# Performance work log

Hardware: AMD Instinct MI355X
Metric: run time of the kernel (lower is better)

The kernel has to match this reference:

```python
import jax, jax.numpy as jnp
import numpy as np

B, N, IN_DIM, HID, OUT, HEADS = 2, 1024, 64, 64, 64, 4
PHD1, PHD2 = HID // HEADS, OUT // HEADS
SLOPE = 0.2  # PyG GATv2Conv default negative_slope
EPS = 1e-12  # F.normalize eps


def _gatv2_dense(x, Wl, Wr, att, bias, heads, phd, mask):
    """Dense GATv2 layer over a full adjacency mask.
    x: [B,N,Din]; Wl/Wr: [Din, heads*phd]; att: [heads,phd]; bias: [heads*phd];
    mask: [N,N] bool, mask[i,j]=True means edge j->i exists.
    """
    Bb, Nn, _ = x.shape
    xl = (x @ Wl).reshape(Bb, Nn, heads, phd)  # source features
    xr = (x @ Wr).reshape(Bb, Nn, heads, phd)  # target features
    # s[b,i,j,h,p] = leaky_relu(xr[b,i] + xl[b,j])  (GATv2)
    s = jax.nn.leaky_relu(xr[:, :, None] + xl[:, None, :], SLOPE)
    e = jnp.einsum('bijhp,hp->bijh', s, att)  # [B,Ni,Nj,H]
    e = jnp.where(mask[None, :, :, None], e, -jnp.inf)
    alpha = jax.nn.softmax(e, axis=2)  # softmax over source nodes j
    out = jnp.einsum('bijh,bjhp->bihp', alpha, xl).reshape(Bb, Nn, heads * phd)
    return out + bias


def setup_inputs() -> dict:
    key = jax.random.key(0)
    ks = jax.random.split(key, 10)
    sc = 0.1
    return {
        'x': jax.random.normal(ks[0], (B, N, IN_DIM), jnp.float32),
        'embedding': jax.random.normal(ks[1], (N, HID), jnp.float32),
        'Wl1': jax.random.normal(ks[2], (IN_DIM, HEADS * PHD1), jnp.float32) * sc,
        'Wr1': jax.random.normal(ks[3], (IN_DIM, HEADS * PHD1), jnp.float32) * sc,
        'att1': jax.random.normal(ks[4], (HEADS, PHD1), jnp.float32) * sc,
        'b1': jnp.zeros((HEADS * PHD1,), jnp.float32),
        'Wl2': jax.random.normal(ks[5], (HID, HEADS * PHD2), jnp.float32) * sc,
        'Wr2': jax.random.normal(ks[6], (HID, HEADS * PHD2), jnp.float32) * sc,
        'att2': jax.random.normal(ks[7], (HEADS, PHD2), jnp.float32) * sc,
        'b2': jnp.zeros((HEADS * PHD2,), jnp.float32),
    }


def reference(x, embedding, Wl1, Wr1, att1, b1, Wl2, Wr2, att2, b2):
    # AdaptiveAdjacency: cosine-similarity adjacency; only its nonzero pattern is used.
    norm = jnp.maximum(jnp.linalg.norm(embedding, axis=1, keepdims=True), EPS)
    ne = embedding / norm
    adj = ne @ ne.T  # [N,N]
    # edge set = adj.nonzero(); GATv2Conv(add_self_loops=True) guarantees diagonal
    mask = (adj != 0) | jnp.eye(N, dtype=bool)
    h = jax.nn.relu(_gatv2_dense(x, Wl1, Wr1, att1, b1, HEADS, PHD1, mask))
    # dropout(0.3) in eval mode -> identity
    return _gatv2_dense(h, Wl2, Wr2, att2, b2, HEADS, PHD2, mask)
```

## Files before the change

### kernel.cpp

```cpp
#include <hip/hip_runtime.h>
#include <math.h>

#define NN 1024
#define BB 2
#define D 64
#define NHEAD 4
#define LOG2E 1.4426950408889634f
#define MST 65

template <int CTRL>
__device__ __forceinline__ float dpp_mov(float x) {
    int xi = __builtin_bit_cast(int, x);
    int r = __builtin_amdgcn_update_dpp(0, xi, CTRL, 0xF, 0xF, true);
    return __builtin_bit_cast(float, r);
}

__device__ __forceinline__ float dpp_rowsum16(float t) {
    t += dpp_mov<0x111>(t);
    t += dpp_mov<0x112>(t);
    t += dpp_mov<0x114>(t);
    t += dpp_mov<0x118>(t);
    return t;
}

__global__ __launch_bounds__(256) void k_mask_gemm(
    const float* __restrict__ emb, unsigned char* __restrict__ mask,
    const float* __restrict__ A, const float* __restrict__ Wl,
    const float* __restrict__ Wr, const float* __restrict__ att,
    float* __restrict__ xl, float* __restrict__ xr, float* __restrict__ alE)
{
    __shared__ float SH[64 * MST * 2];
    int tid = threadIdx.x;
    if (blockIdx.x < 256) {
        float* As = SH;
        float* Bs = SH + 64 * MST;
        int ib = (blockIdx.x & 15) << 6;
        int jb = (blockIdx.x >> 4) << 6;

        #pragma unroll
        for (int r = 0; r < 4; ++r) {
            int q = tid + (r << 8);
            int row = q >> 4, c4 = (q & 15) << 2;
            float4 a = *(const float4*)&emb[(ib + row) * D + c4];
            float4 b = *(const float4*)&emb[(jb + row) * D + c4];
            As[row * MST + c4 + 0] = a.x; As[row * MST + c4 + 1] = a.y;
            As[row * MST + c4 + 2] = a.z; As[row * MST + c4 + 3] = a.w;
            Bs[row * MST + c4 + 0] = b.x; Bs[row * MST + c4 + 1] = b.y;
            Bs[row * MST + c4 + 2] = b.z; Bs[row * MST + c4 + 3] = b.w;
        }
        __syncthreads();

        int i0 = (tid >> 4) << 2;
        int j0 = (tid & 15) << 2;
        float acc[4][4] = {};
        #pragma unroll 8
        for (int k = 0; k < 64; ++k) {
            float a0 = As[(i0 + 0) * MST + k];
            float a1 = As[(i0 + 1) * MST + k];
            float a2 = As[(i0 + 2) * MST + k];
            float a3 = As[(i0 + 3) * MST + k];
            float b0 = Bs[(j0 + 0) * MST + k];
            float b1 = Bs[(j0 + 1) * MST + k];
            float b2 = Bs[(j0 + 2) * MST + k];
            float b3 = Bs[(j0 + 3) * MST + k];
            acc[0][0] = fmaf(a0, b0, acc[0][0]); acc[0][1] = fmaf(a0, b1, acc[0][1]);
            acc[0][2] = fmaf(a0, b2, acc[0][2]); acc[0][3] = fmaf(a0, b3, acc[0][3]);
            acc[1][0] = fmaf(a1, b0, acc[1][0]); acc[1][1] = fmaf(a1, b1, acc[1][1]);
            acc[1][2] = fmaf(a1, b2, acc[1][2]); acc[1][3] = fmaf(a1, b3, acc[1][3]);
            acc[2][0] = fmaf(a2, b0, acc[2][0]); acc[2][1] = fmaf(a2, b1, acc[2][1]);
            acc[2][2] = fmaf(a2, b2, acc[2][2]); acc[2][3] = fmaf(a2, b3, acc[2][3]);
            acc[3][0] = fmaf(a3, b0, acc[3][0]); acc[3][1] = fmaf(a3, b1, acc[3][1]);
            acc[3][2] = fmaf(a3, b2, acc[3][2]); acc[3][3] = fmaf(a3, b3, acc[3][3]);
        }
        #pragma unroll
        for (int r = 0; r < 4; ++r) {
            int gi = ib + i0 + r;
            uchar4 m;
            m.x = (acc[r][0] != 0.f || gi == jb + j0 + 0) ? 1 : 0;
            m.y = (acc[r][1] != 0.f || gi == jb + j0 + 1) ? 1 : 0;
            m.z = (acc[r][2] != 0.f || gi == jb + j0 + 2) ? 1 : 0;
            m.w = (acc[r][3] != 0.f || gi == jb + j0 + 3) ? 1 : 0;
            *(uchar4*)&mask[gi * NN + jb + j0] = m;
        }
    } else {
        float* wl = SH;
        float* wr = SH + 4096;
        for (int t = tid; t < 4096; t += 256) { wl[t] = Wl[t]; wr[t] = Wr[t]; }
        __syncthreads();
        int r = (blockIdx.x - 256) * 4 + (tid >> 6);
        int c = tid & 63;
        float av = att[c];
        const float* arow = A + r * 64;
        float accl = 0.f, accr = 0.f;
        #pragma unroll
        for (int p = 0; p < 64; ++p) {
            float a = arow[p];
            accl = fmaf(a, wl[p * 64 + c], accl);
            accr = fmaf(a, wr[p * 64 + c], accr);
        }
        int cp = (((c >> 2) & 3) << 4) | ((c >> 4) << 2) | (c & 3);
        xl[r * 64 + cp] = accl;
        xr[r * 64 + c] = accr;
        float t = dpp_rowsum16(accl * av);
        if ((c & 15) == 15) alE[(r << 2) | (c >> 4)] = 0.6f * LOG2E * t;
    }
}

__global__ __launch_bounds__(256) void k_gemm2(const float* __restrict__ A,
                                               const float* __restrict__ Wl,
                                               const float* __restrict__ Wr,
                                               const float* __restrict__ att,
                                               float* __restrict__ xl,
                                               float* __restrict__ xr,
                                               float* __restrict__ alE) {
    __shared__ float wl[64 * 64];
    __shared__ float wr[64 * 64];
    int tid = threadIdx.x;
    for (int t = tid; t < 4096; t += 256) { wl[t] = Wl[t]; wr[t] = Wr[t]; }
    __syncthreads();
    int r = blockIdx.x * 4 + (tid >> 6);
    int c = tid & 63;
    float av = att[c];
    const float* arow = A + r * 64;
    float accl = 0.f, accr = 0.f;
    #pragma unroll
    for (int p = 0; p < 64; ++p) {
        float a = arow[p];
        accl = fmaf(a, wl[p * 64 + c], accl);
        accr = fmaf(a, wr[p * 64 + c], accr);
    }
    int cp = (((c >> 2) & 3) << 4) | ((c >> 4) << 2) | (c & 3);
    xl[r * 64 + cp] = accl;
    xr[r * 64 + c] = accr;
    float t = dpp_rowsum16(accl * av);
    if ((c & 15) == 15) alE[(r << 2) | (c >> 4)] = 0.6f * LOG2E * t;
}

template <bool RELU>
__global__ __launch_bounds__(256, 2) void k_attn(
    const float* __restrict__ xlp, const float* __restrict__ xr,
    const float* __restrict__ att, const float* __restrict__ alE,
    const float* __restrict__ bias, const unsigned char* __restrict__ mask,
    float* __restrict__ out)
{
    __shared__ float Opart[4][4][4][64];
    __shared__ float Lpart[4][4][4][NHEAD];

    int tid = threadIdx.x;
    int wave = tid >> 6, lane = tid & 63;
    int h = lane & 3, jl = lane >> 2;
    int b = blockIdx.x >> 8;
    int i0 = (blockIdx.x & 255) << 2;
    int j0 = (wave << 8) + (jl << 4);

    const float* xlb = xlp + (b << 16);

    float at[16], xr0f[16], xr1f[16], xr2f[16], xr3f[16];
    {
        const float* ap = att + (h << 4);
        const float* r0 = xr + (((b << 10) + i0) << 6) + (h << 4);
        const float* r1 = r0 + 64;
        const float* r2 = r0 + 128;
        const float* r3 = r0 + 192;
        #pragma unroll
        for (int c = 0; c < 4; ++c) {
            *(float4*)&at[c << 2]   = *(const float4*)(ap + (c << 2));
            *(float4*)&xr0f[c << 2] = *(const float4*)(r0 + (c << 2));
            *(float4*)&xr1f[c << 2] = *(const float4*)(r1 + (c << 2));
            *(float4*)&xr2f[c << 2] = *(const float4*)(r2 + (c << 2));
            *(float4*)&xr3f[c << 2] = *(const float4*)(r3 + (c << 2));
        }
        #pragma unroll
        for (int p = 0; p < 16; ++p) at[p] *= 0.4f * LOG2E;
    }
    float ar0, ar1, ar2, ar3;
    {
        float s0[4], s1[4], s2[4], s3[4];
        #pragma unroll
        for (int c = 0; c < 4; ++c) {
            float t0 = 0.f, t1 = 0.f, t2 = 0.f, t3 = 0.f;
            #pragma unroll
            for (int r = 0; r < 4; ++r) {
                int p = (c << 2) + r;
                float a = at[p];
                t0 = fmaf(a, xr0f[p], t0);
                t1 = fmaf(a, xr1f[p], t1);
                t2 = fmaf(a, xr2f[p], t2);
                t3 = fmaf(a, xr3f[p], t3);
            }
            s0[c] = t0; s1[c] = t1; s2[c] = t2; s3[c] = t3;
        }
        ar0 = 1.5f * ((s0[0] + s0[1]) + (s0[2] + s0[3]));
        ar1 = 1.5f * ((s1[0] + s1[1]) + (s1[2] + s1[3]));
        ar2 = 1.5f * ((s2[0] + s2[1]) + (s2[2] + s2[3]));
        ar3 = 1.5f * ((s3[0] + s3[1]) + (s3[2] + s3[3]));
    }

    unsigned mb0 = 0, mb1 = 0, mb2 = 0, mb3 = 0;
    {
        const unsigned* m0p = (const unsigned*)(mask + (i0 + 0) * NN + j0);
        const unsigned* m1p = (const unsigned*)(mask + (i0 + 1) * NN + j0);
        const unsigned* m2p = (const unsigned*)(mask + (i0 + 2) * NN + j0);
        const unsigned* m3p = (const unsigned*)(mask + (i0 + 3) * NN + j0);
        #pragma unroll
        for (int q = 0; q < 4; ++q) {
            unsigned w0 = m0p[q], w1 = m1p[q], w2 = m2p[q], w3 = m3p[q];
            mb0 |= ((((w0 >> 0) & 1) | ((w0 >> 7) & 2) | ((w0 >> 14) & 4) | ((w0 >> 21) & 8)) << (q << 2));
            mb1 |= ((((w1 >> 0) & 1) | ((w1 >> 7) & 2) | ((w1 >> 14) & 4) | ((w1 >> 21) & 8)) << (q << 2));
            mb2 |= ((((w2 >> 0) & 1) | ((w2 >> 7) & 2) | ((w2 >> 14) & 4) | ((w2 >> 21) & 8)) << (q << 2));
            mb3 |= ((((w3 >> 0) & 1) | ((w3 >> 7) & 2) | ((w3 >> 14) & 4) | ((w3 >> 21) & 8)) << (q << 2));
        }
    }

    float O0[16], O1[16], O2[16], O3[16];
    float lq0 = 0.f, lq1 = 0.f, lq2 = 0.f, lq3 = 0.f;
    #pragma unroll
    for (int p = 0; p < 16; ++p) { O0[p] = 0.f; O1[p] = 0.f; O2[p] = 0.f; O3[p] = 0.f; }

    const float* xrow = xlb + (j0 << 6) + (h << 2);
    const float* alp  = alE + (b << 12) + (j0 << 2) + h;

    #pragma unroll 2
    for (int s = 0; s < 16; ++s) {
        const float* rp = xrow + (s << 6);
        float xv[16];
        *(float4*)&xv[0]  = *(const float4*)(rp);
        *(float4*)&xv[4]  = *(const float4*)(rp + 16);
        *(float4*)&xv[8]  = *(const float4*)(rp + 32);
        *(float4*)&xv[12] = *(const float4*)(rp + 48);
        float alr = alp[s << 2];
        bool m0 = (mb0 >> s) & 1, m1 = (mb1 >> s) & 1;
        bool m2 = (mb2 >> s) & 1, m3 = (mb3 >> s) & 1;

        float s0[4], s1[4], s2[4], s3[4];
        #pragma unroll
        for (int c = 0; c < 4; ++c) {
            float t0 = 0.f, t1 = 0.f, t2 = 0.f, t3 = 0.f;
            #pragma unroll
            for (int r = 0; r < 4; ++r) {
                int p = (c << 2) + r;
                float a = at[p], xvv = xv[p];
                t0 = fmaf(a, __builtin_fabsf(xr0f[p] + xvv), t0);
                t1 = fmaf(a, __builtin_fabsf(xr1f[p] + xvv), t1);
                t2 = fmaf(a, __builtin_fabsf(xr2f[p] + xvv), t2);
                t3 = fmaf(a, __builtin_fabsf(xr3f[p] + xvv), t3);
            }
            s0[c] = t0; s1[c] = t1; s2[c] = t2; s3[c] = t3;
        }
        float e0 = ((s0[0] + s0[1]) + (s0[2] + s0[3])) + (ar0 + alr);
        float e1 = ((s1[0] + s1[1]) + (s1[2] + s1[3])) + (ar1 + alr);
        float e2 = ((s2[0] + s2[1]) + (s2[2] + s2[3])) + (ar2 + alr);
        float e3 = ((s3[0] + s3[1]) + (s3[2] + s3[3])) + (ar3 + alr);
        float pe0 = m0 ? __builtin_amdgcn_exp2f(e0) : 0.f;
        float pe1 = m1 ? __builtin_amdgcn_exp2f(e1) : 0.f;
        float pe2 = m2 ? __builtin_amdgcn_exp2f(e2) : 0.f;
        float pe3 = m3 ? __builtin_amdgcn_exp2f(e3) : 0.f;
        lq0 += pe0; lq1 += pe1; lq2 += pe2; lq3 += pe3;
        #pragma unroll
        for (int p = 0; p < 16; ++p) {
            float xvv = xv[p];
            O0[p] = fmaf(pe0, xvv, O0[p]);
            O1[p] = fmaf(pe1, xvv, O1[p]);
            O2[p] = fmaf(pe2, xvv, O2[p]);
            O3[p] = fmaf(pe3, xvv, O3[p]);
        }
    }

    #pragma unroll
    for (int p = 0; p < 16; ++p) {
        O0[p] += dpp_mov<0x114>(O0[p]);  O0[p] += dpp_mov<0x118>(O0[p]);
        O1[p] += dpp_mov<0x114>(O1[p]);  O1[p] += dpp_mov<0x118>(O1[p]);
        O2[p] += dpp_mov<0x114>(O2[p]);  O2[p] += dpp_mov<0x118>(O2[p]);
        O3[p] += dpp_mov<0x114>(O3[p]);  O3[p] += dpp_mov<0x118>(O3[p]);
    }
    lq0 += dpp_mov<0x114>(lq0);  lq0 += dpp_mov<0x118>(lq0);
    lq1 += dpp_mov<0x114>(lq1);  lq1 += dpp_mov<0x118>(lq1);
    lq2 += dpp_mov<0x114>(lq2);  lq2 += dpp_mov<0x118>(lq2);
    lq3 += dpp_mov<0x114>(lq3);  lq3 += dpp_mov<0x118>(lq3);

    if ((lane & 15) >= 12) {
        int k = lane >> 4;
        #pragma unroll
        for (int c = 0; c < 4; ++c) {
            *(float4*)&Opart[0][wave][k][(h << 4) + (c << 2)] = *(const float4*)&O0[c << 2];
            *(float4*)&Opart[1][wave][k][(h << 4) + (c << 2)] = *(const float4*)&O1[c << 2];
            *(float4*)&Opart[2][wave][k][(h << 4) + (c << 2)] = *(const float4*)&O2[c << 2];
            *(float4*)&Opart[3][wave][k][(h << 4) + (c << 2)] = *(const float4*)&O3[c << 2];
        }
        Lpart[0][wave][k][h] = lq0;
        Lpart[1][wave][k][h] = lq1;
        Lpart[2][wave][k][h] = lq2;
        Lpart[3][wave][k][h] = lq3;
    }
    __syncthreads();

    {
        int ii = tid >> 6, c = tid & 63;
        float o = 0.f, l = 0.f;
        #pragma unroll
        for (int w = 0; w < 4; ++w)
            #pragma unroll
            for (int k = 0; k < 4; ++k) {
                o += Opart[ii][w][k][c];
                l += Lpart[ii][w][k][c >> 4];
            }
        float res = o / l + bias[c];
        if (RELU) res = fmaxf(res, 0.f);
        out[((b << 10) + i0 + ii) * D + c] = res;
    }
}

extern "C" void kernel_launch(void* const* d_in, const int* in_sizes, int n_in,
                              void* d_out, int out_size, void* d_ws, size_t ws_size,
                              hipStream_t stream) {
    const float* x    = (const float*)d_in[0];
    const float* emb  = (const float*)d_in[1];
    const float* Wl1  = (const float*)d_in[2];
    const float* Wr1  = (const float*)d_in[3];
    const float* att1 = (const float*)d_in[4];
    const float* b1   = (const float*)d_in[5];
    const float* Wl2  = (const float*)d_in[6];
    const float* Wr2  = (const float*)d_in[7];
    const float* att2 = (const float*)d_in[8];
    const float* b2   = (const float*)d_in[9];
    float* out = (float*)d_out;

    unsigned char* mask = (unsigned char*)d_ws;
    float* xl = (float*)(mask + NN * NN);
    float* xr = xl + BB * NN * D;
    float* hbuf = xr + BB * NN * D;
    float* alE = hbuf + BB * NN * D;

    k_mask_gemm<<<256 + BB * NN / 4, 256, 0, stream>>>(emb, mask, x, Wl1, Wr1, att1, xl, xr, alE);
    k_attn<true><<<BB * NN / 4, 256, 0, stream>>>(xl, xr, att1, alE, b1, mask, hbuf);

    k_gemm2<<<BB * NN / 4, 256, 0, stream>>>(hbuf, Wl2, Wr2, att2, xl, xr, alE);
    k_attn<false><<<BB * NN / 4, 256, 0, stream>>>(xl, xr, att2, alE, b2, mask, out);
}
```

Measured before the change: 130.4 us.

## Fuse layer-2 projection GEMM into the layer-1 attention epilogue

Removes the separate k_gemm2 launch. The layer-1 attention kernel now keeps its ReLU output rows in shared memory and multiplies them by Wl2/Wr2, which are staged into 32KB of extra LDS. It then writes xl2, xr2 and alE2 directly, skipping the hbuf round trip through global memory and one kernel launch. The extra LDS per block may reduce occupancy of the attention kernel under launch_bounds(256,2), and layer-1 outputs now go to separate buffers.

```diff
diff --git a/kernel.cpp b/kernel.cpp
--- a/kernel.cpp
+++ b/kernel.cpp
@@ -106,45 +106,20 @@
     }
 }
 
-__global__ __launch_bounds__(256) void k_gemm2(const float* __restrict__ A,
-                                               const float* __restrict__ Wl,
-                                               const float* __restrict__ Wr,
-                                               const float* __restrict__ att,
-                                               float* __restrict__ xl,
-                                               float* __restrict__ xr,
-                                               float* __restrict__ alE) {
-    __shared__ float wl[64 * 64];
-    __shared__ float wr[64 * 64];
-    int tid = threadIdx.x;
-    for (int t = tid; t < 4096; t += 256) { wl[t] = Wl[t]; wr[t] = Wr[t]; }
-    __syncthreads();
-    int r = blockIdx.x * 4 + (tid >> 6);
-    int c = tid & 63;
-    float av = att[c];
-    const float* arow = A + r * 64;
-    float accl = 0.f, accr = 0.f;
-    #pragma unroll
-    for (int p = 0; p < 64; ++p) {
-        float a = arow[p];
-        accl = fmaf(a, wl[p * 64 + c], accl);
-        accr = fmaf(a, wr[p * 64 + c], accr);
-    }
-    int cp = (((c >> 2) & 3) << 4) | ((c >> 4) << 2) | (c & 3);
-    xl[r * 64 + cp] = accl;
-    xr[r * 64 + c] = accr;
-    float t = dpp_rowsum16(accl * av);
-    if ((c & 15) == 15) alE[(r << 2) | (c >> 4)] = 0.6f * LOG2E * t;
-}
-
-template <bool RELU>
+template <bool RELU, bool FUSEG>
 __global__ __launch_bounds__(256, 2) void k_attn(
     const float* __restrict__ xlp, const float* __restrict__ xr,
     const float* __restrict__ att, const float* __restrict__ alE,
     const float* __restrict__ bias, const unsigned char* __restrict__ mask,
-    float* __restrict__ out)
+    float* __restrict__ out,
+    const float* __restrict__ Wl2, const float* __restrict__ Wr2,
+    const float* __restrict__ att2,
+    float* __restrict__ xl2, float* __restrict__ xr2, float* __restrict__ alE2)
 {
     __shared__ float Opart[4][4][4][64];
     __shared__ float Lpart[4][4][4][NHEAD];
+    __shared__ float SHW[FUSEG ? 8192 : 1];
+    __shared__ float RES[FUSEG ? 4 : 1][64];
 
     int tid = threadIdx.x;
     int wave = tid >> 6, lane = tid & 63;
@@ -152,6 +127,10 @@
     int b = blockIdx.x >> 8;
     int i0 = (blockIdx.x & 255) << 2;
     int j0 = (wave << 8) + (jl << 4);
+
+    if constexpr (FUSEG) {
+        for (int t = tid; t < 4096; t += 256) { SHW[t] = Wl2[t]; SHW[4096 + t] = Wr2[t]; }
+    }
 
     const float* xlb = xlp + (b << 16);
 
@@ -306,7 +285,31 @@
             }
         float res = o / l + bias[c];
         if (RELU) res = fmaxf(res, 0.f);
-        out[((b << 10) + i0 + ii) * D + c] = res;
+        if constexpr (FUSEG) {
+            RES[ii][c] = res;
+        } else {
+            out[((b << 10) + i0 + ii) * D + c] = res;
+        }
+    }
+
+    if constexpr (FUSEG) {
+        __syncthreads();
+        int ii = tid >> 6, c = tid & 63;
+        int rr = (blockIdx.x << 2) + ii;
+        float av = att2[c];
+        const float* arow = &RES[ii][0];
+        float accl = 0.f, accr = 0.f;
+        #pragma unroll
+        for (int p = 0; p < 64; ++p) {
+            float a = arow[p];
+            accl = fmaf(a, SHW[p * 64 + c], accl);
+            accr = fmaf(a, SHW[4096 + p * 64 + c], accr);
+        }
+        int cp = (((c >> 2) & 3) << 4) | ((c >> 4) << 2) | (c & 3);
+        xl2[rr * 64 + cp] = accl;
+        xr2[rr * 64 + c] = accr;
+        float t = dpp_rowsum16(accl * av);
+        if ((c & 15) == 15) alE2[(rr << 2) | (c >> 4)] = 0.6f * LOG2E * t;
     }
 }
 
@@ -326,14 +329,20 @@
     float* out = (float*)d_out;
 
     unsigned char* mask = (unsigned char*)d_ws;
-    float* xl = (float*)(mask + NN * NN);
-    float* xr = xl + BB * NN * D;
-    float* hbuf = xr + BB * NN * D;
-    float* alE = hbuf + BB * NN * D;
+    float* xl   = (float*)(mask + NN * NN);
+    float* xr   = xl + BB * NN * D;
+    float* xl2  = xr + BB * NN * D;
+    float* alE  = xl2 + BB * NN * D;
+    float* xr2  = alE + BB * NN * NHEAD;
+    float* alE2 = xr2 + BB * NN * D;
 
     k_mask_gemm<<<256 + BB * NN / 4, 256, 0, stream>>>(emb, mask, x, Wl1, Wr1, att1, xl, xr, alE);
-    k_attn<true><<<BB * NN / 4, 256, 0, stream>>>(xl, xr, att1, alE, b1, mask, hbuf);
-
-    k_gemm2<<<BB * NN / 4, 256, 0, stream>>>(hbuf, Wl2, Wr2, att2, xl, xr, alE);
-    k_attn<false><<<BB * NN / 4, 256, 0, stream>>>(xl, xr, att2, alE, b2, mask, out);
-}
+
+    k_attn<true, true><<<BB * NN / 4, 256, 0, stream>>>(
+        xl, xr, att1, alE, b1, mask, xl2 ,
+        Wl2, Wr2, att2, xl2, xr2, alE2);
+
+    k_attn<false, false><<<BB * NN / 4, 256, 0, stream>>>(
+        xl2, xr2, att2, alE2, b2, mask, out,
+        Wl2, Wr2, att2, xl2, xr2, alE2 );
+}
```

Result: no change. 128.2 us (-1.7%).
